# Kernel tuning notes

Measured on AMD Instinct MI355X. Metric: run time of the kernel, lower is better.

## Reference

```python
import jax, jax.numpy as jnp
import numpy as np

EMBED_DIM = 1024
N_HEADS = 16
HEAD_DIM = EMBED_DIM // N_HEADS


def setup_inputs() -> dict:
    key = jax.random.key(0)
    k1, k2, k3 = jax.random.split(key, 3)
    B, T, D = 2, 2048, EMBED_DIM
    x = jax.random.normal(k1, (B, T, D), dtype=jnp.float32)
    # torch nn.Linear weights: (out_features, in_features); y = x @ W.T
    scale = 1.0 / np.sqrt(D)
    qkv_w = jax.random.uniform(k2, (3 * D, D), dtype=jnp.float32, minval=-scale, maxval=scale)
    out_w = jax.random.uniform(k3, (D, D), dtype=jnp.float32, minval=-scale, maxval=scale)
    return {"x": x, "qkv_w": qkv_w, "out_w": out_w}


def reference(x, qkv_w, out_w):
    B, T, D = x.shape
    H, hd = N_HEADS, HEAD_DIM
    qkv = jnp.einsum('btd,ed->bte', x, qkv_w)  # (B,T,3D)
    qkv = qkv.reshape(B, T, 3, H, hd)
    q = jnp.transpose(qkv[:, :, 0], (0, 2, 1, 3))  # (B,H,T,hd)
    k = jnp.transpose(qkv[:, :, 1], (0, 2, 1, 3))
    v = jnp.transpose(qkv[:, :, 2], (0, 2, 1, 3))
    scores = jnp.einsum('bhtd,bhsd->bhts', q, k) / np.sqrt(hd).astype(np.float32)
    causal = jnp.tril(jnp.ones((T, T), dtype=bool))  # True = keep
    scores = jnp.where(causal[None, None], scores, -jnp.inf)
    probs = jax.nn.softmax(scores, axis=-1)
    out = jnp.einsum('bhts,bhsd->bhtd', probs, v)
    out = jnp.transpose(out, (0, 2, 1, 3)).reshape(B, T, D)
    return jnp.einsum('btd,ed->bte', out, out_w)
```

## Files before the change

### kernel.cpp

```cpp
#include <hip/hip_runtime.h>
#include <hip/hip_bf16.h>
#include <stdint.h>

typedef __bf16 bf16;
typedef __attribute__((ext_vector_type(8))) __bf16 bf16x8;
typedef __attribute__((ext_vector_type(4))) __bf16 bf16x4;
typedef __attribute__((ext_vector_type(4))) float f32x4;

#define AS1 __attribute__((address_space(1)))
#define AS3 __attribute__((address_space(3)))

__device__ __forceinline__ void async16(const void* g, void* l) {
  __builtin_amdgcn_global_load_lds((AS1 uint32_t*)(g), (AS3 uint32_t*)(l), 16, 0, 0);
}

__device__ __forceinline__ f32x4 mfma_bf16(bf16x8 a, bf16x8 b, f32x4 c) {
  return __builtin_amdgcn_mfma_f32_16x16x32_bf16(a, b, c, 0, 0, 0);
}

__device__ __forceinline__ uint32_t pack2_bf16(float a, float b) {
  union { __hip_bfloat162 h2; uint32_t u; } u;
  u.h2 = __float22bfloat162_rn(float2{a, b});
  return u.u;
}

__global__ __launch_bounds__(256) void cast_all_kernel(
    const float* __restrict__ x, const float* __restrict__ w1,
    const float* __restrict__ w2, bf16* __restrict__ xb,
    bf16* __restrict__ w1b, bf16* __restrict__ w2b) {
  const int bid = blockIdx.x;
  const float* src;
  bf16* dst;
  int base;
  if (bid < 4096) { src = x;  dst = xb;  base = bid; }
  else if (bid < 7168) { src = w1; dst = w1b; base = bid - 4096; }
  else { src = w2; dst = w2b; base = bid - 7168; }
  const int i = (base * 256 + threadIdx.x) * 4;
  const float4 v = *(const float4*)(src + i);
  bf16x4 o;
  o[0] = (bf16)v.x; o[1] = (bf16)v.y; o[2] = (bf16)v.z; o[3] = (bf16)v.w;
  *(bf16x4*)(dst + i) = o;
}

__global__ __launch_bounds__(256) void gemm_qkv_kernel(
    const bf16* __restrict__ A, const bf16* __restrict__ W,
    bf16* __restrict__ QK, bf16* __restrict__ VT) {
  constexpr int K = 1024;
  __shared__ __align__(16) bf16 sm[2 * 128 * 32];
  const int tid = threadIdx.x;
  const int w = tid >> 6, lane = tid & 63;
  const int m0 = blockIdx.x * 128, n0 = blockIdx.y * 128;
  const int wm = (w >> 1) * 64, wn = (w & 1) * 64;
  const int lrow = lane & 15, quad = lane >> 4;
  const int lk = quad * 8;
  f32x4 acc[4][4] = {};

  for (int k0 = 0; k0 < K; k0 += 32) {
#pragma unroll
    for (int i = 0; i < 4; ++i) {
      const int c = tid + 256 * i;
      const bf16* src = (c < 512)
          ? (A + (size_t)(m0 + (c >> 2)) * K + k0 + (c & 3) * 8)
          : (W + (size_t)(n0 + ((c - 512) >> 2)) * K + k0 + (c & 3) * 8);
      async16(src, sm + (w * 64 + i * 256) * 8);
    }
    __syncthreads();
    bf16x8 af[4], bfr[4];
#pragma unroll
    for (int mi = 0; mi < 4; ++mi)
      af[mi] = *(const bf16x8*)&sm[(wm + mi * 16 + lrow) * 32 + lk];
#pragma unroll
    for (int ni = 0; ni < 4; ++ni)
      bfr[ni] = *(const bf16x8*)&sm[128 * 32 + (wn + ni * 16 + lrow) * 32 + lk];
#pragma unroll
    for (int mi = 0; mi < 4; ++mi)
#pragma unroll
      for (int ni = 0; ni < 4; ++ni)
        acc[mi][ni] = mfma_bf16(af[mi], bfr[ni], acc[mi][ni]);
    __syncthreads();
  }

  bf16* s2 = sm;
  const bool isV = (n0 >= 2048);
  const int bb = m0 >> 11;
  const int mt = m0 & 2047;
  if (!isV) {
#pragma unroll
    for (int c = 0; c < 2; ++c) {
      if ((w >> 1) == c) {
#pragma unroll
        for (int mi = 0; mi < 4; ++mi)
#pragma unroll
          for (int ni = 0; ni < 4; ++ni) {
            const int nr = wn + ni * 16 + lrow;
#pragma unroll
            for (int r = 0; r < 4; ++r)
              s2[(mi * 16 + quad * 4 + r) * 128 + nr] = (bf16)acc[mi][ni][r];
          }
      }
      __syncthreads();
#pragma unroll
      for (int p = 0; p < 4; ++p) {
        const int row = p * 16 + (tid >> 4);
        const int colc = (tid & 15) * 8;
        const bf16x8 v = *(const bf16x8*)&s2[row * 128 + colc];
        *(bf16x8*)(QK + (size_t)(m0 + c * 64 + row) * 2048 + n0 + colc) = v;
      }
      __syncthreads();
    }
  } else {
#pragma unroll
    for (int c = 0; c < 2; ++c) {
      if ((w & 1) == c) {
#pragma unroll
        for (int mi = 0; mi < 4; ++mi)
#pragma unroll
          for (int ni = 0; ni < 4; ++ni) {
            const int nl = ni * 16 + lrow;
            bf16x4 pk4;
#pragma unroll
            for (int r = 0; r < 4; ++r) pk4[r] = (bf16)acc[mi][ni][r];
            *(bf16x4*)&s2[nl * 128 + wm + mi * 16 + quad * 4] = pk4;
          }
      }
      __syncthreads();
#pragma unroll
      for (int p = 0; p < 4; ++p) {
        const int row = p * 16 + (tid >> 4);
        const int colc = (tid & 15) * 8;
        const bf16x8 v = *(const bf16x8*)&s2[row * 128 + colc];
        const int vtrow = bb * 1024 + (n0 - 2048) + c * 64 + row;
        *(bf16x8*)(VT + (size_t)vtrow * 2048 + mt + colc) = v;
      }
      __syncthreads();
    }
  }
}

__global__ __launch_bounds__(256) void attn_kernel(
    const bf16* __restrict__ QK, const bf16* __restrict__ VT,
    bf16* __restrict__ AO) {
  __shared__ __align__(16) bf16 sK[2][64 * 64];
  __shared__ __align__(16) bf16 sV[2][64 * 64];
  const int bh = blockIdx.x;
  const int qt = 31 - blockIdx.y;
  const int b = bh >> 4, h = bh & 15;
  const int tid = threadIdx.x, w = tid >> 6, lane = tid & 63;
  const int qhalf = w >> 1, parity = w & 1;
  const int q0 = qt * 64;
  const int col = lane & 15, quad = lane >> 4;
  const bf16* Qb = QK + (size_t)b * 2048 * 2048 + h * 64;
  const bf16* Kb = Qb + 1024;
  const bf16* Vb = VT + (size_t)bh * 64 * 2048;
  const float NEG_INF = -__builtin_inff();
  constexpr float QSCALE = 0.18033688011112042f;

  union { uint32_t u[4]; bf16x8 v; } ones;
  ones.u[0] = 0x3F803F80u; ones.u[1] = 0x3F803F80u;
  ones.u[2] = 0x3F803F80u; ones.u[3] = 0x3F803F80u;

  int qrow[2];
  bf16x8 qf[2][2];
#pragma unroll
  for (int qtile = 0; qtile < 2; ++qtile) {
    qrow[qtile] = q0 + qhalf * 32 + qtile * 16 + col;
#pragma unroll
    for (int kk = 0; kk < 2; ++kk) {
      bf16x8 v = *(const bf16x8*)(Qb + (size_t)qrow[qtile] * 2048 + kk * 32 + quad * 8);
#pragma unroll
      for (int e = 0; e < 8; ++e) v[e] = (bf16)((float)v[e] * QSCALE);
      qf[qtile][kk] = v;
    }
  }

  auto stage = [&](int s0) {
#pragma unroll
    for (int i = 0; i < 4; ++i) {
      const int L = tid + 256 * i;
      const int buf = L >> 9, Lr = L & 511;
      const int row = Lr >> 3;
      const int ch = (Lr & 7) ^ (row & 7);
      async16(Kb + (size_t)(s0 + buf * 64 + row) * 2048 + ch * 8, &sK[0][L * 8]);
    }
#pragma unroll
    for (int i = 0; i < 4; ++i) {
      const int L = tid + 256 * i;
      const int buf = L >> 9, Lr = L & 511;
      const int d = Lr >> 3;
      const int ch = (Lr & 7) ^ (d & 7);
      async16(Vb + (size_t)d * 2048 + s0 + buf * 64 + ch * 8, &sV[0][L * 8]);
    }
  };

  int srow[4];
#pragma unroll
  for (int m = 0; m < 4; ++m)
    srow[m] = 32 * (m & 1) + (col >> 2) * 8 + 4 * (m >> 1) + (col & 3);

  f32x4 accO[4][2] = {};
  f32x4 accL[2] = {};

  auto body = [&](int kt, bool masked) {
    const int s0 = kt * 64;
    const bf16* kbuf = &sK[0][parity * 4096];
    const bf16* vbuf = &sV[0][parity * 4096];

    f32x4 st[2][4] = {};
#pragma unroll
    for (int kk = 0; kk < 2; ++kk) {
      bf16x8 kf[4];
#pragma unroll
      for (int m = 0; m < 4; ++m)
        kf[m] = *(const bf16x8*)&kbuf[srow[m] * 64 + (((kk * 4 + quad) ^ (srow[m] & 7)) * 8)];
#pragma unroll
      for (int m = 0; m < 4; ++m)
#pragma unroll
        for (int qtile = 0; qtile < 2; ++qtile)
          st[qtile][m] = mfma_bf16(kf[m], qf[qtile][kk], st[qtile][m]);
    }

    if (masked) {
#pragma unroll
      for (int qtile = 0; qtile < 2; ++qtile)
#pragma unroll
        for (int m = 0; m < 4; ++m) {
          const int kvb = s0 + 32 * (m & 1) + quad * 8 + 4 * (m >> 1);
#pragma unroll
          for (int r = 0; r < 4; ++r)
            st[qtile][m][r] = (kvb + r <= qrow[qtile]) ? st[qtile][m][r] : NEG_INF;
        }
    }

    uint32_t pk[2][4][2];
#pragma unroll
    for (int qtile = 0; qtile < 2; ++qtile)
#pragma unroll
      for (int m = 0; m < 4; ++m) {
        const float p0 = __builtin_amdgcn_exp2f(st[qtile][m][0]);
        const float p1 = __builtin_amdgcn_exp2f(st[qtile][m][1]);
        const float p2 = __builtin_amdgcn_exp2f(st[qtile][m][2]);
        const float p3 = __builtin_amdgcn_exp2f(st[qtile][m][3]);
        pk[qtile][m][0] = pack2_bf16(p0, p1);
        pk[qtile][m][1] = pack2_bf16(p2, p3);
      }

#pragma unroll
    for (int kk = 0; kk < 2; ++kk) {
      bf16x8 vf[4];
#pragma unroll
      for (int d = 0; d < 4; ++d) {
        const int row = d * 16 + col;
        vf[d] = *(const bf16x8*)&vbuf[row * 64 + (((kk * 4 + quad) ^ (row & 7)) * 8)];
      }
#pragma unroll
      for (int qtile = 0; qtile < 2; ++qtile) {
        union { uint32_t u[4]; bf16x8 v; } f;
        f.u[0] = pk[qtile][kk][0];
        f.u[1] = pk[qtile][kk][1];
        f.u[2] = pk[qtile][2 + kk][0];
        f.u[3] = pk[qtile][2 + kk][1];
        accL[qtile] = mfma_bf16(ones.v, f.v, accL[qtile]);
#pragma unroll
        for (int d = 0; d < 4; ++d)
          accO[d][qtile] = mfma_bf16(vf[d], f.v, accO[d][qtile]);
      }
    }
  };

  const int npairs = (qt >> 1) + 1;
  for (int j = 0; j < npairs; ++j) {
    stage(j * 128);
    __syncthreads();
    const int kt = 2 * j + parity;
    if (kt <= qt) body(kt, kt == qt);
    __syncthreads();
  }

  float* scrO = (float*)sK;
  float* scrL = (float*)sV;
  if (parity == 1) {
    const int base = qhalf * 2048;
#pragma unroll
    for (int d = 0; d < 4; ++d)
#pragma unroll
      for (int qtile = 0; qtile < 2; ++qtile)
#pragma unroll
        for (int r = 0; r < 4; ++r)
          scrO[base + ((d * 2 + qtile) * 4 + r) * 64 + lane] = accO[d][qtile][r];
#pragma unroll
    for (int qtile = 0; qtile < 2; ++qtile)
      scrL[qhalf * 128 + qtile * 64 + lane] = accL[qtile][0];
  }
  __syncthreads();
  if (parity == 0) {
    const int base = qhalf * 2048;
#pragma unroll
    for (int d = 0; d < 4; ++d)
#pragma unroll
      for (int qtile = 0; qtile < 2; ++qtile)
#pragma unroll
        for (int r = 0; r < 4; ++r)
          accO[d][qtile][r] += scrO[base + ((d * 2 + qtile) * 4 + r) * 64 + lane];
    bf16* Ob = AO + (size_t)b * 2048 * 1024 + h * 64;
#pragma unroll
    for (int qtile = 0; qtile < 2; ++qtile) {
      const float inv = 1.0f / (accL[qtile][0] + scrL[qhalf * 128 + qtile * 64 + lane]);
#pragma unroll
      for (int d = 0; d < 4; ++d) {
        bf16x4 o;
#pragma unroll
        for (int r = 0; r < 4; ++r) o[r] = (bf16)(accO[d][qtile][r] * inv);
        *(bf16x4*)(Ob + (size_t)qrow[qtile] * 1024 + d * 16 + quad * 4) = o;
      }
    }
  }
}

__global__ __launch_bounds__(256) void gemm_out_kernel(
    const bf16* __restrict__ A, const bf16* __restrict__ W,
    float* __restrict__ C) {
  constexpr int K = 1024;
  __shared__ __align__(16) bf16 sm[2 * 128 * 32];
  const int tid = threadIdx.x;
  const int w = tid >> 6, lane = tid & 63;
  const int m0 = blockIdx.x * 128, n0 = blockIdx.y * 128;
  const int wm = (w >> 1) * 64, wn = (w & 1) * 64;
  const int lrow = lane & 15, lk = (lane >> 4) * 8;
  f32x4 acc[4][4] = {};

  for (int k0 = 0; k0 < K; k0 += 32) {
#pragma unroll
    for (int i = 0; i < 4; ++i) {
      const int c = tid + 256 * i;
      const bf16* src = (c < 512)
          ? (A + (size_t)(m0 + (c >> 2)) * K + k0 + (c & 3) * 8)
          : (W + (size_t)(n0 + ((c - 512) >> 2)) * K + k0 + (c & 3) * 8);
      async16(src, sm + (w * 64 + i * 256) * 8);
    }
    __syncthreads();
    bf16x8 af[4], bfr[4];
#pragma unroll
    for (int mi = 0; mi < 4; ++mi)
      af[mi] = *(const bf16x8*)&sm[(wm + mi * 16 + lrow) * 32 + lk];
#pragma unroll
    for (int ni = 0; ni < 4; ++ni)
      bfr[ni] = *(const bf16x8*)&sm[128 * 32 + (wn + ni * 16 + lrow) * 32 + lk];
#pragma unroll
    for (int mi = 0; mi < 4; ++mi)
#pragma unroll
      for (int ni = 0; ni < 4; ++ni)
        acc[mi][ni] = mfma_bf16(af[mi], bfr[ni], acc[mi][ni]);
    __syncthreads();
  }

#pragma unroll
  for (int mi = 0; mi < 4; ++mi)
#pragma unroll
    for (int ni = 0; ni < 4; ++ni) {
      const int n = n0 + wn + ni * 16 + lrow;
#pragma unroll
      for (int r = 0; r < 4; ++r) {
        const int m = m0 + wm + mi * 16 + (lane >> 4) * 4 + r;
        C[(size_t)m * 1024 + n] = acc[mi][ni][r];
      }
    }
}

extern "C" void kernel_launch(void* const* d_in, const int* in_sizes, int n_in,
                              void* d_out, int out_size, void* d_ws, size_t ws_size,
                              hipStream_t stream) {
  const float* x     = (const float*)d_in[0];
  const float* qkv_w = (const float*)d_in[1];
  const float* out_w = (const float*)d_in[2];
  float* out = (float*)d_out;

  char* ws = (char*)d_ws;
  bf16* xb    = (bf16*)(ws);
  bf16* aob   = (bf16*)(ws);
  bf16* wqkvb = (bf16*)(ws + 8u * 1024 * 1024);
  bf16* wob   = (bf16*)(ws + 14u * 1024 * 1024);
  bf16* qkb   = (bf16*)(ws + 16u * 1024 * 1024);
  bf16* vtb   = (bf16*)(ws + 32u * 1024 * 1024);

  cast_all_kernel<<<8192, 256, 0, stream>>>(x, qkv_w, out_w, xb, wqkvb, wob);
  gemm_qkv_kernel<<<dim3(32, 24), 256, 0, stream>>>(xb, wqkvb, qkb, vtb);
  attn_kernel<<<dim3(32, 32), 256, 0, stream>>>(qkb, vtb, aob);
  gemm_out_kernel<<<dim3(32, 8), 256, 0, stream>>>(aob, wob, out);
}
```

Measured before the change: 170.3 us.

## Double-buffer K/V staging in attention, remap blocks per XCD, add MFMA priority

The attention kernel now keeps two LDS buffers for K and V and prefetches the next key pair while computing the current one. This replaces the load-then-compute pattern that had a barrier before and after each step. The grid becomes 1D with a mapping that keeps four (batch, head) pairs on each XCD, aiming for better L2 reuse of K/V. s_setprio is raised around the MFMA blocks. The cost is doubled LDS use (64KB), which may reduce occupancy, and the raw s_waitcnt plus s_barrier ordering must stay correct.

```diff
diff --git a/kernel.cpp b/kernel.cpp
--- a/kernel.cpp
+++ b/kernel.cpp
@@ -140,10 +140,12 @@
 __global__ __launch_bounds__(256) void attn_kernel(
     const bf16* __restrict__ QK, const bf16* __restrict__ VT,
     bf16* __restrict__ AO) {
-  __shared__ __align__(16) bf16 sK[2][64 * 64];
-  __shared__ __align__(16) bf16 sV[2][64 * 64];
-  const int bh = blockIdx.x;
-  const int qt = 31 - blockIdx.y;
+  __shared__ __align__(16) bf16 sK[2][2][64 * 64];
+  __shared__ __align__(16) bf16 sV[2][2][64 * 64];
+  const int bid = blockIdx.x;
+  const int xcd = bid & 7, slot = bid >> 3;
+  const int bh = xcd * 4 + (slot & 3);
+  const int qt = 31 - (slot >> 2);
   const int b = bh >> 4, h = bh & 15;
   const int tid = threadIdx.x, w = tid >> 6, lane = tid & 63;
   const int qhalf = w >> 1, parity = w & 1;
@@ -173,14 +175,16 @@
     }
   }
 
-  auto stage = [&](int s0) {
+  auto stage = [&](int s0, int cur) {
+    bf16* dK = &sK[cur][0][0];
+    bf16* dV = &sV[cur][0][0];
 #pragma unroll
     for (int i = 0; i < 4; ++i) {
       const int L = tid + 256 * i;
       const int buf = L >> 9, Lr = L & 511;
       const int row = Lr >> 3;
       const int ch = (Lr & 7) ^ (row & 7);
-      async16(Kb + (size_t)(s0 + buf * 64 + row) * 2048 + ch * 8, &sK[0][L * 8]);
+      async16(Kb + (size_t)(s0 + buf * 64 + row) * 2048 + ch * 8, dK + L * 8);
     }
 #pragma unroll
     for (int i = 0; i < 4; ++i) {
@@ -188,7 +192,7 @@
       const int buf = L >> 9, Lr = L & 511;
       const int d = Lr >> 3;
       const int ch = (Lr & 7) ^ (d & 7);
-      async16(Vb + (size_t)d * 2048 + s0 + buf * 64 + ch * 8, &sV[0][L * 8]);
+      async16(Vb + (size_t)d * 2048 + s0 + buf * 64 + ch * 8, dV + L * 8);
     }
   };
 
@@ -200,10 +204,10 @@
   f32x4 accO[4][2] = {};
   f32x4 accL[2] = {};
 
-  auto body = [&](int kt, bool masked) {
+  auto body = [&](int kt, bool masked, int cur) {
     const int s0 = kt * 64;
-    const bf16* kbuf = &sK[0][parity * 4096];
-    const bf16* vbuf = &sV[0][parity * 4096];
+    const bf16* kbuf = &sK[cur][parity][0];
+    const bf16* vbuf = &sV[cur][parity][0];
 
     f32x4 st[2][4] = {};
 #pragma unroll
@@ -212,11 +216,13 @@
 #pragma unroll
       for (int m = 0; m < 4; ++m)
         kf[m] = *(const bf16x8*)&kbuf[srow[m] * 64 + (((kk * 4 + quad) ^ (srow[m] & 7)) * 8)];
+      __builtin_amdgcn_s_setprio(1);
 #pragma unroll
       for (int m = 0; m < 4; ++m)
 #pragma unroll
         for (int qtile = 0; qtile < 2; ++qtile)
           st[qtile][m] = mfma_bf16(kf[m], qf[qtile][kk], st[qtile][m]);
+      __builtin_amdgcn_s_setprio(0);
     }
 
     if (masked) {
@@ -252,6 +258,7 @@
         const int row = d * 16 + col;
         vf[d] = *(const bf16x8*)&vbuf[row * 64 + (((kk * 4 + quad) ^ (row & 7)) * 8)];
       }
+      __builtin_amdgcn_s_setprio(1);
 #pragma unroll
       for (int qtile = 0; qtile < 2; ++qtile) {
         union { uint32_t u[4]; bf16x8 v; } f;
@@ -264,16 +271,22 @@
         for (int d = 0; d < 4; ++d)
           accO[d][qtile] = mfma_bf16(vf[d], f.v, accO[d][qtile]);
       }
+      __builtin_amdgcn_s_setprio(0);
     }
   };
 
   const int npairs = (qt >> 1) + 1;
+  stage(0, 0);
+  asm volatile("s_waitcnt vmcnt(0)" ::: "memory");
+  __builtin_amdgcn_s_barrier();
+  int cur = 0;
   for (int j = 0; j < npairs; ++j) {
-    stage(j * 128);
-    __syncthreads();
+    if (j + 1 < npairs) stage((j + 1) * 128, cur ^ 1);
     const int kt = 2 * j + parity;
-    if (kt <= qt) body(kt, kt == qt);
-    __syncthreads();
+    if (kt <= qt) body(kt, kt == qt, cur);
+    asm volatile("s_waitcnt vmcnt(0)" ::: "memory");
+    __builtin_amdgcn_s_barrier();
+    cur ^= 1;
   }
 
   float* scrO = (float*)sK;
@@ -384,6 +397,6 @@
 
   cast_all_kernel<<<8192, 256, 0, stream>>>(x, qkv_w, out_w, xb, wqkvb, wob);
   gemm_qkv_kernel<<<dim3(32, 24), 256, 0, stream>>>(xb, wqkvb, qkb, vtb);
-  attn_kernel<<<dim3(32, 32), 256, 0, stream>>>(qkb, vtb, aob);
+  attn_kernel<<<dim3(1024), 256, 0, stream>>>(qkb, vtb, aob);
   gemm_out_kernel<<<dim3(32, 8), 256, 0, stream>>>(aob, wob, out);
 }
```

Result: no change. 172.5 us (+1.3%).
